# Kernel tuning notes

Hardware: AMD Instinct MI355X
Metric: run time of the kernel (lower is better)

The kernel has to match this reference:

```python
import jax, jax.numpy as jnp
import numpy as np

H_DIM = 1024
GATE_DIM = 128


def setup_inputs() -> dict:
    key = jax.random.key(0)
    ks = jax.random.split(key, 7)
    B, L = 32, 2048
    bound_g = 1.0 / np.sqrt(GATE_DIM)
    bound_l = 1.0 / np.sqrt(GATE_DIM)
    return {
        "x": jax.random.normal(ks[0], (B, L, H_DIM), dtype=jnp.float32),
        # GRUCell params (PyTorch layout: rows ordered [r; z; n])
        "weight_ih": jax.random.uniform(ks[1], (3 * GATE_DIM, H_DIM), minval=-bound_g, maxval=bound_g, dtype=jnp.float32),
        "weight_hh": jax.random.uniform(ks[2], (3 * GATE_DIM, GATE_DIM), minval=-bound_g, maxval=bound_g, dtype=jnp.float32),
        "bias_ih": jax.random.uniform(ks[3], (3 * GATE_DIM,), minval=-bound_g, maxval=bound_g, dtype=jnp.float32),
        "bias_hh": jax.random.uniform(ks[4], (3 * GATE_DIM,), minval=-bound_g, maxval=bound_g, dtype=jnp.float32),
        # output linear (gate_dim -> 1)
        "lin_w": jax.random.uniform(ks[5], (1, GATE_DIM), minval=-bound_l, maxval=bound_l, dtype=jnp.float32),
        "lin_b": jax.random.uniform(ks[6], (1,), minval=-bound_l, maxval=bound_l, dtype=jnp.float32),
    }


def reference(x, weight_ih, weight_hh, bias_ih, bias_hh, lin_w, lin_b):
    """Faithful to the original PingHead.forward: `s` is never updated, so every
    timestep runs the GRUCell against a ZERO hidden state. weight_hh @ h == 0,
    leaving only bias_hh contributions. This lets us vectorize over (B, L)."""
    G = GATE_DIM
    # input projection for all gates: (B, L, 3G)
    gi = jnp.einsum('blh,gh->blg', x, weight_ih) + bias_ih
    i_r, i_z, i_n = gi[..., :G], gi[..., G:2 * G], gi[..., 2 * G:]
    b_hr, b_hz, b_hn = bias_hh[:G], bias_hh[G:2 * G], bias_hh[2 * G:]
    r = jax.nn.sigmoid(i_r + b_hr)
    z = jax.nn.sigmoid(i_z + b_hz)
    n = jnp.tanh(i_n + r * b_hn)
    h = (1.0 - z) * n  # + z * 0 (hidden state is always zero)
    # linear(gate_dim -> 1), squeeze last dim -> (B, L)
    out = jnp.einsum('blg,og->blo', h, lin_w) + lin_b
    return out[..., 0]
```

## Files before the change

kernel.cpp:

```cpp
#include <hip/hip_runtime.h>

#define H_DIM   1024
#define G_DIM   128
#define N_DIM   384
#define M_TOTAL 65536
#define BM      64
#define LDA     72
#define ABUF    (BM * LDA)

typedef _Float16 half8  __attribute__((ext_vector_type(8)));
typedef __fp16   fp16x2 __attribute__((ext_vector_type(2)));
typedef float    f32x4  __attribute__((ext_vector_type(4)));

__device__ __forceinline__ float fast_sigmoid(float v) {
    return 1.0f / (1.0f + __expf(-v));
}
__device__ __forceinline__ float fast_tanh(float v) {
    return 1.0f - 2.0f / (__expf(2.0f * v) + 1.0f);
}

__device__ __forceinline__ half8 cvt8(f32x4 a, f32x4 b) {
    fp16x2 p0 = __builtin_amdgcn_cvt_pkrtz(a[0], a[1]);
    fp16x2 p1 = __builtin_amdgcn_cvt_pkrtz(a[2], a[3]);
    fp16x2 p2 = __builtin_amdgcn_cvt_pkrtz(b[0], b[1]);
    fp16x2 p3 = __builtin_amdgcn_cvt_pkrtz(b[2], b[3]);
    half8 h;
    h[0] = (_Float16)p0[0]; h[1] = (_Float16)p0[1];
    h[2] = (_Float16)p1[0]; h[3] = (_Float16)p1[1];
    h[4] = (_Float16)p2[0]; h[5] = (_Float16)p2[1];
    h[6] = (_Float16)p3[0]; h[7] = (_Float16)p3[1];
    return h;
}

__global__ __launch_bounds__(256) void prep_w_kernel(const float* __restrict__ w,
                                                     _Float16* __restrict__ wf) {
    int gid  = blockIdx.x * 256 + threadIdx.x;
    int lane = gid & 63;
    int fid  = gid >> 6;
    int ktg  = fid & 31;
    int ct   = fid >> 5;
    int col  = ct * 16 + (lane & 15);
    int kb   = ktg * 32 + (lane >> 4) * 8;
    const f32x4* src = (const f32x4*)(w + (size_t)col * H_DIM + kb);
    f32x4 v0 = src[0], v1 = src[1];
    half8 h;
    #pragma unroll
    for (int j = 0; j < 4; ++j) { h[j] = (_Float16)v0[j]; h[4 + j] = (_Float16)v1[j]; }
    *(half8*)(wf + (size_t)gid * 8) = h;
}

__global__ __launch_bounds__(256) void ping_main_kernel(
    const float* __restrict__ x, const _Float16* __restrict__ wf,
    const float* __restrict__ bias_ih, const float* __restrict__ bias_hh,
    const float* __restrict__ lin_w, const float* __restrict__ lin_b,
    float* __restrict__ out)
{
    __shared__ _Float16 shA[2 * ABUF];
    __shared__ float sh_out[BM];

    const int t    = threadIdx.x;
    const int lane = t & 63;
    const int wv   = t >> 6;
    const int ln   = lane & 15;
    const int quad = lane >> 4;

    if (t < BM) sh_out[t] = 0.0f;

    const size_t row0 = (size_t)blockIdx.x * BM;

    f32x4 acc[6][4];
    #pragma unroll
    for (int i = 0; i < 6; ++i)
        #pragma unroll
        for (int rt = 0; rt < 4; ++rt)
            acc[i][rt] = (f32x4){0.f, 0.f, 0.f, 0.f};

    const int rs = t >> 2;
    const int kg = (t & 3) * 16;
    const float* xptr = x + (row0 + rs) * (size_t)H_DIM + kg;
    _Float16* sW0 = &shA[rs * LDA + kg];
    _Float16* sW1 = sW0 + ABUF;

    const _Float16* pb[6];
    #pragma unroll
    for (int i = 0; i < 6; ++i) {
        const int ct = ((i >> 1) * 8) + 2 * wv + (i & 1);
        pb[i] = wf + ((size_t)(ct * 32) * 64 + lane) * 8;
    }

    f32x4 q0, q1, q2, q3;
    { const f32x4* s = (const f32x4*)xptr; q0 = s[0]; q1 = s[1]; q2 = s[2]; q3 = s[3]; xptr += 64; }
    *(half8*)sW0       = cvt8(q0, q1);
    *(half8*)(sW0 + 8) = cvt8(q2, q3);
    __syncthreads();

    #pragma unroll
    for (int kb = 0; kb < 16; ++kb) {
        const bool pref = (kb < 15);
        if (pref) { const f32x4* s = (const f32x4*)xptr; q0 = s[0]; q1 = s[1]; q2 = s[2]; q3 = s[3]; xptr += 64; }

        const _Float16* aRd = (kb & 1) ? (shA + ABUF) : shA;
        #pragma unroll
        for (int kt = 0; kt < 2; ++kt) {
            half8 b[6];
            #pragma unroll
            for (int i = 0; i < 6; ++i)
                b[i] = *(const half8*)(pb[i] + kt * 512);
            half8 a[4];
            #pragma unroll
            for (int rt = 0; rt < 4; ++rt)
                a[rt] = *(const half8*)(aRd + (rt * 16 + ln) * LDA + kt * 32 + quad * 8);
            #pragma unroll
            for (int i = 0; i < 6; ++i)
                #pragma unroll
                for (int rt = 0; rt < 4; ++rt)
                    acc[i][rt] = __builtin_amdgcn_mfma_f32_16x16x32_f16(a[rt], b[i], acc[i][rt], 0, 0, 0);
        }
        #pragma unroll
        for (int i = 0; i < 6; ++i) pb[i] += 1024;

        if (pref) {
            _Float16* w = (kb & 1) ? sW0 : sW1;
            *(half8*)w       = cvt8(q0, q1);
            *(half8*)(w + 8) = cvt8(q2, q3);
        }
        __syncthreads();
    }

    float psum[4][4];
    #pragma unroll
    for (int rt = 0; rt < 4; ++rt)
        #pragma unroll
        for (int reg = 0; reg < 4; ++reg)
            psum[rt][reg] = 0.f;

    #pragma unroll
    for (int i = 0; i < 2; ++i) {
        const int g = 32 * wv + 16 * i + ln;
        const float b_ir = bias_ih[g];
        const float b_iz = bias_ih[G_DIM + g];
        const float b_in = bias_ih[2 * G_DIM + g];
        const float b_hr = bias_hh[g];
        const float b_hz = bias_hh[G_DIM + g];
        const float b_hn = bias_hh[2 * G_DIM + g];
        const float lw   = lin_w[g];
        #pragma unroll
        for (int rt = 0; rt < 4; ++rt) {
            #pragma unroll
            for (int reg = 0; reg < 4; ++reg) {
                const float r = fast_sigmoid(acc[i][rt][reg] + b_ir + b_hr);
                const float z = fast_sigmoid(acc[2 + i][rt][reg] + b_iz + b_hz);
                const float n = fast_tanh(acc[4 + i][rt][reg] + b_in + r * b_hn);
                psum[rt][reg] += lw * (1.0f - z) * n;
            }
        }
    }

    #pragma unroll
    for (int rt = 0; rt < 4; ++rt) {
        #pragma unroll
        for (int reg = 0; reg < 4; ++reg) {
            float v = psum[rt][reg];
            v += __shfl_xor(v, 1);
            v += __shfl_xor(v, 2);
            v += __shfl_xor(v, 4);
            v += __shfl_xor(v, 8);
            if (ln == 0) atomicAdd(&sh_out[rt * 16 + quad * 4 + reg], v);
        }
    }

    __syncthreads();
    if (t < BM) out[row0 + t] = sh_out[t] + lin_b[0];
}

extern "C" void kernel_launch(void* const* d_in, const int* in_sizes, int n_in,
                              void* d_out, int out_size, void* d_ws, size_t ws_size,
                              hipStream_t stream) {
    const float* x      = (const float*)d_in[0];
    const float* w_ih   = (const float*)d_in[1];
    const float* b_ih   = (const float*)d_in[3];
    const float* b_hh   = (const float*)d_in[4];
    const float* lin_w  = (const float*)d_in[5];
    const float* lin_b  = (const float*)d_in[6];
    float* out          = (float*)d_out;
    _Float16* wf        = (_Float16*)d_ws;

    hipLaunchKernelGGL(prep_w_kernel, dim3((N_DIM / 16) * 32 * 64 / 256), dim3(256), 0, stream,
                       w_ih, wf);
    hipLaunchKernelGGL(ping_main_kernel, dim3(M_TOTAL / BM), dim3(256), 0, stream,
                       x, wf, b_ih, b_hh, lin_w, lin_b, out);
}
```

Before: 469.7 us.

## Stream x into LDS via async global_load_lds with 4-stage pipeline and 8 waves

Replaces the register-staged fp32 load plus fp16 convert-and-store into LDS with direct global-to-LDS async loads of raw fp32 x into a 4-deep ring buffer with an XOR swizzle. The fp16 conversion moves to read time from LDS. Block size doubles to 512 threads so each wave owns one 16-column tile per gate, which cuts accumulators and raises occupancy. The aim is more memory-level parallelism on this bandwidth-bound x stream, at the cost of more LDS traffic (fp32), conversion work repeated on every read, and hand-written waitcnt/barrier synchronisation.

```diff
diff --git a/kernel.cpp b/kernel.cpp
--- a/kernel.cpp
+++ b/kernel.cpp
@@ -5,8 +5,8 @@
 #define N_DIM   384
 #define M_TOTAL 65536
 #define BM      64
-#define LDA     72
-#define ABUF    (BM * LDA)
+#define NSTEP   32
+#define BUF_FLOATS 2048
 
 typedef _Float16 half8  __attribute__((ext_vector_type(8)));
 typedef __fp16   fp16x2 __attribute__((ext_vector_type(2)));
@@ -49,13 +49,17 @@
     *(half8*)(wf + (size_t)gid * 8) = h;
 }
 
-__global__ __launch_bounds__(256) void ping_main_kernel(
+#define FENCE() asm volatile("" ::: "memory")
+#define WAITV(N) { FENCE(); __builtin_amdgcn_s_waitcnt(0x0F70 | (N)); FENCE(); }
+#define BARR()   { FENCE(); __builtin_amdgcn_s_barrier(); FENCE(); }
+
+__global__ __launch_bounds__(512, 4) void ping_main_kernel(
     const float* __restrict__ x, const _Float16* __restrict__ wf,
     const float* __restrict__ bias_ih, const float* __restrict__ bias_hh,
     const float* __restrict__ lin_w, const float* __restrict__ lin_b,
     float* __restrict__ out)
 {
-    __shared__ _Float16 shA[2 * ABUF];
+    __shared__ float shX[4 * BUF_FLOATS];
     __shared__ float sh_out[BM];
 
     const int t    = threadIdx.x;
@@ -68,99 +72,85 @@
 
     const size_t row0 = (size_t)blockIdx.x * BM;
 
-    f32x4 acc[6][4];
+    const int drow = wv * 8 + (lane >> 3);
+    const int cg   = (lane & 7) ^ (2 * ((lane >> 3) & 3));
+    const float* xsrc = x + (row0 + drow) * (size_t)H_DIM + cg * 4;
+    float* ldsSeg = &shX[wv * 256];
+
+#define DMA_ISSUE(K) \
+    __builtin_amdgcn_global_load_lds( \
+        (const __attribute__((address_space(1))) void*)(xsrc + (size_t)(K) * 32), \
+        (__attribute__((address_space(3))) void*)(ldsSeg + ((K) & 3) * BUF_FLOATS), \
+        16, 0, 0)
+
+    const char* aAddr[4];
     #pragma unroll
-    for (int i = 0; i < 6; ++i)
+    for (int rt = 0; rt < 4; ++rt) {
+        int r  = rt * 16 + ln;
+        int ce = (2 * quad) ^ (2 * (ln & 3));
+        aAddr[rt] = (const char*)&shX[0] + r * 128 + ce * 16;
+    }
+
+    const _Float16* pb[3];
+    #pragma unroll
+    for (int i = 0; i < 3; ++i)
+        pb[i] = wf + (size_t)((wv + 8 * i) * 32) * 512 + lane * 8;
+
+    f32x4 acc[3][4];
+    #pragma unroll
+    for (int i = 0; i < 3; ++i)
         #pragma unroll
         for (int rt = 0; rt < 4; ++rt)
             acc[i][rt] = (f32x4){0.f, 0.f, 0.f, 0.f};
 
-    const int rs = t >> 2;
-    const int kg = (t & 3) * 16;
-    const float* xptr = x + (row0 + rs) * (size_t)H_DIM + kg;
-    _Float16* sW0 = &shA[rs * LDA + kg];
-    _Float16* sW1 = sW0 + ABUF;
+    DMA_ISSUE(0); DMA_ISSUE(1); DMA_ISSUE(2);
 
-    const _Float16* pb[6];
-    #pragma unroll
-    for (int i = 0; i < 6; ++i) {
-        const int ct = ((i >> 1) * 8) + 2 * wv + (i & 1);
-        pb[i] = wf + ((size_t)(ct * 32) * 64 + lane) * 8;
+#define ITER_BODY(KB, BUFI, WAITN, DO_ISSUE) { \
+    WAITV(WAITN); \
+    BARR(); \
+    if (DO_ISSUE) { DMA_ISSUE((KB) + 3); } \
+    half8 bfr[3]; \
+    _Pragma("unroll") \
+    for (int i = 0; i < 3; ++i) \
+        bfr[i] = *(const half8*)(pb[i] + (size_t)(KB) * 512); \
+    _Pragma("unroll") \
+    for (int rt = 0; rt < 4; ++rt) { \
+        f32x4 ve = *(const f32x4*)(aAddr[rt] + (BUFI) * 8192); \
+        f32x4 vo = *(const f32x4*)(aAddr[rt] + (BUFI) * 8192 + 16); \
+        half8 afr = cvt8(ve, vo); \
+        _Pragma("unroll") \
+        for (int i = 0; i < 3; ++i) \
+            acc[i][rt] = __builtin_amdgcn_mfma_f32_16x16x32_f16(afr, bfr[i], acc[i][rt], 0, 0, 0); \
+    } }
+
+    for (int kb = 0; kb < 28; kb += 4) {
+        ITER_BODY(kb + 0, 0, 2, true);
+        ITER_BODY(kb + 1, 1, 2, true);
+        ITER_BODY(kb + 2, 2, 2, true);
+        ITER_BODY(kb + 3, 3, 2, true);
     }
+    ITER_BODY(28, 0, 2, true);
+    ITER_BODY(29, 1, 2, false);
+    ITER_BODY(30, 2, 1, false);
+    ITER_BODY(31, 3, 0, false);
 
-    f32x4 q0, q1, q2, q3;
-    { const f32x4* s = (const f32x4*)xptr; q0 = s[0]; q1 = s[1]; q2 = s[2]; q3 = s[3]; xptr += 64; }
-    *(half8*)sW0       = cvt8(q0, q1);
-    *(half8*)(sW0 + 8) = cvt8(q2, q3);
-    __syncthreads();
-
-    #pragma unroll
-    for (int kb = 0; kb < 16; ++kb) {
-        const bool pref = (kb < 15);
-        if (pref) { const f32x4* s = (const f32x4*)xptr; q0 = s[0]; q1 = s[1]; q2 = s[2]; q3 = s[3]; xptr += 64; }
-
-        const _Float16* aRd = (kb & 1) ? (shA + ABUF) : shA;
-        #pragma unroll
-        for (int kt = 0; kt < 2; ++kt) {
-            half8 b[6];
-            #pragma unroll
-            for (int i = 0; i < 6; ++i)
-                b[i] = *(const half8*)(pb[i] + kt * 512);
-            half8 a[4];
-            #pragma unroll
-            for (int rt = 0; rt < 4; ++rt)
-                a[rt] = *(const half8*)(aRd + (rt * 16 + ln) * LDA + kt * 32 + quad * 8);
-            #pragma unroll
-            for (int i = 0; i < 6; ++i)
-                #pragma unroll
-                for (int rt = 0; rt < 4; ++rt)
-                    acc[i][rt] = __builtin_amdgcn_mfma_f32_16x16x32_f16(a[rt], b[i], acc[i][rt], 0, 0, 0);
-        }
-        #pragma unroll
-        for (int i = 0; i < 6; ++i) pb[i] += 1024;
-
-        if (pref) {
-            _Float16* w = (kb & 1) ? sW0 : sW1;
-            *(half8*)w       = cvt8(q0, q1);
-            *(half8*)(w + 8) = cvt8(q2, q3);
-        }
-        __syncthreads();
-    }
-
-    float psum[4][4];
-    #pragma unroll
-    for (int rt = 0; rt < 4; ++rt)
-        #pragma unroll
-        for (int reg = 0; reg < 4; ++reg)
-            psum[rt][reg] = 0.f;
-
-    #pragma unroll
-    for (int i = 0; i < 2; ++i) {
-        const int g = 32 * wv + 16 * i + ln;
-        const float b_ir = bias_ih[g];
-        const float b_iz = bias_ih[G_DIM + g];
-        const float b_in = bias_ih[2 * G_DIM + g];
-        const float b_hr = bias_hh[g];
-        const float b_hz = bias_hh[G_DIM + g];
-        const float b_hn = bias_hh[2 * G_DIM + g];
-        const float lw   = lin_w[g];
-        #pragma unroll
-        for (int rt = 0; rt < 4; ++rt) {
-            #pragma unroll
-            for (int reg = 0; reg < 4; ++reg) {
-                const float r = fast_sigmoid(acc[i][rt][reg] + b_ir + b_hr);
-                const float z = fast_sigmoid(acc[2 + i][rt][reg] + b_iz + b_hz);
-                const float n = fast_tanh(acc[4 + i][rt][reg] + b_in + r * b_hn);
-                psum[rt][reg] += lw * (1.0f - z) * n;
-            }
-        }
-    }
+    const int g = 16 * wv + ln;
+    const float b_ir = bias_ih[g];
+    const float b_iz = bias_ih[G_DIM + g];
+    const float b_in = bias_ih[2 * G_DIM + g];
+    const float b_hr = bias_hh[g];
+    const float b_hz = bias_hh[G_DIM + g];
+    const float b_hn = bias_hh[2 * G_DIM + g];
+    const float lw   = lin_w[g];
 
     #pragma unroll
     for (int rt = 0; rt < 4; ++rt) {
         #pragma unroll
         for (int reg = 0; reg < 4; ++reg) {
-            float v = psum[rt][reg];
+            const float r = fast_sigmoid(acc[0][rt][reg] + b_ir + b_hr);
+            const float z = fast_sigmoid(acc[1][rt][reg] + b_iz + b_hz);
+            const float n = fast_tanh(acc[2][rt][reg] + b_in + r * b_hn);
+            float v = lw * (1.0f - z) * n;
             v += __shfl_xor(v, 1);
             v += __shfl_xor(v, 2);
             v += __shfl_xor(v, 4);
@@ -187,6 +177,6 @@
 
     hipLaunchKernelGGL(prep_w_kernel, dim3((N_DIM / 16) * 32 * 64 / 256), dim3(256), 0, stream,
                        w_ih, wf);
-    hipLaunchKernelGGL(ping_main_kernel, dim3(M_TOTAL / BM), dim3(256), 0, stream,
+    hipLaunchKernelGGL(ping_main_kernel, dim3(M_TOTAL / BM), dim3(512), 0, stream,
                        x, wf, b_ih, b_hh, lin_w, lin_b, out);
 }
```

Measured after the change: 408.1 us. 1.15x faster.
